# Kernel optimization log

Measured on AMD Instinct MI355X. Metric: run time of the kernel, lower is better.

## Reference

```python
import jax, jax.numpy as jnp
import numpy as np

HIDDEN = 2048
NUM_HEADS = 16
HEAD_DIM = HIDDEN // NUM_HEADS
ROPE_THETA = 10000.0
B, S = 2, 2048
NEG_INF = jnp.finfo(jnp.float32).min


def _rope_tables(seq_len, head_dim, base):
    inv_freq = 1.0 / (base ** (jnp.arange(0, head_dim, 2, dtype=jnp.float32) / head_dim))
    t = jnp.arange(seq_len, dtype=jnp.float32)
    freqs = jnp.outer(t, inv_freq)                 # [S, head_dim/2]
    emb = jnp.concatenate([freqs, freqs], axis=-1) # [S, head_dim]
    return jnp.cos(emb), jnp.sin(emb)


def _rotate_half(x):
    x1, x2 = jnp.split(x, 2, axis=-1)
    return jnp.concatenate([-x2, x1], axis=-1)


def _apply_rope(q, k, cos, sin, position_ids):
    # q,k: [B,H,S,D]; cos/sin: [S_max,D]; position_ids: [B,S]
    c = cos[position_ids][:, None, :, :]  # [B,1,S,D]
    s = sin[position_ids][:, None, :, :]
    q = q * c + _rotate_half(q) * s
    k = k * c + _rotate_half(k) * s
    return q, k


def setup_inputs() -> dict:
    key = jax.random.key(0)
    ks = jax.random.split(key, 5)
    hidden_states = jax.random.normal(ks[0], (B, S, HIDDEN), dtype=jnp.float32)
    # causal additive mask, shape (B,1,S,S)
    causal = jnp.triu(jnp.full((S, S), NEG_INF, dtype=jnp.float32), k=1)
    attention_mask = jnp.broadcast_to(causal[None, None], (B, 1, S, S))
    position_ids = jnp.broadcast_to(jnp.arange(S, dtype=jnp.int32)[None], (B, S))
    scale = 1.0 / np.sqrt(HIDDEN)
    Wq = jax.random.normal(ks[1], (HIDDEN, HIDDEN), dtype=jnp.float32) * scale
    Wk = jax.random.normal(ks[2], (HIDDEN, HIDDEN), dtype=jnp.float32) * scale
    Wv = jax.random.normal(ks[3], (HIDDEN, HIDDEN), dtype=jnp.float32) * scale
    Wo = jax.random.normal(ks[4], (HIDDEN, HIDDEN), dtype=jnp.float32) * scale
    return {"hidden_states": hidden_states, "attention_mask": attention_mask,
            "position_ids": position_ids, "Wq": Wq, "Wk": Wk, "Wv": Wv, "Wo": Wo}


def reference(hidden_states, attention_mask, position_ids, Wq, Wk, Wv, Wo):
    bsz, q_len, _ = hidden_states.shape
    def proj(W):
        # nn.Linear: x @ W.T -> [B,S,H*D] -> [B,H,S,D]
        y = jnp.einsum('bse,fe->bsf', hidden_states, W)
        return y.reshape(bsz, q_len, NUM_HEADS, HEAD_DIM).transpose(0, 2, 1, 3)
    q, k, v = proj(Wq), proj(Wk), proj(Wv)
    cos, sin = _rope_tables(q_len, HEAD_DIM, ROPE_THETA)
    q, k = _apply_rope(q, k, cos, sin, position_ids)
    scores = jnp.einsum('bhqd,bhkd->bhqk', q, k) / np.sqrt(HEAD_DIM)
    scores = scores + attention_mask
    scores = jnp.maximum(scores, NEG_INF)
    weights = jax.nn.softmax(scores.astype(jnp.float32), axis=-1).astype(q.dtype)
    attn = jnp.einsum('bhqk,bhkd->bhqd', weights, v)
    attn = attn.transpose(0, 2, 1, 3).reshape(bsz, q_len, HIDDEN)
    return jnp.einsum('bsf,ef->bse', attn, Wo)
```

## Files before the change

kernel.cpp:

```cpp
#include <hip/hip_runtime.h>
#include <hip/hip_bf16.h>

typedef __attribute__((ext_vector_type(4))) float f32x4;
typedef __attribute__((ext_vector_type(8))) short bf16x8;
typedef __attribute__((ext_vector_type(4))) unsigned u32x4;

__device__ __forceinline__ short f2b(float f) {
  unsigned u = __builtin_bit_cast(unsigned, f);
  u += 0x7FFFu + ((u >> 16) & 1u);
  return (short)(u >> 16);
}
__device__ __forceinline__ float b2f(short s) {
  unsigned u = ((unsigned)(unsigned short)s) << 16;
  return __builtin_bit_cast(float, u);
}
__device__ __forceinline__ unsigned cvtpk(float lo, float hi) {
  unsigned r;
  asm("v_cvt_pk_bf16_f32 %0, %1, %2" : "=v"(r) : "v"(lo), "v"(hi));
  return r;
}

__device__ __forceinline__ void async16(const void* g, void* l) {
  __builtin_amdgcn_global_load_lds(
      (const __attribute__((address_space(1))) void*)g,
      (__attribute__((address_space(3))) void*)l, 16, 0, 0);
}

#define BM 128
#define BN 128
#define BK 64

__global__ __launch_bounds__(256) void cvt_kernel(
    const float* __restrict__ X, const float* __restrict__ Wq,
    const float* __restrict__ Wk, const float* __restrict__ Wv,
    const float* __restrict__ Wo, short* __restrict__ dst) {
  const size_t u = (size_t)blockIdx.x * 256 + threadIdx.x;
  const float* src;
  short* d;
  size_t off;
  if (u < 1048576) {
    src = X; d = dst; off = u * 8;
  } else {
    const size_t j = u - 1048576;
    const int ten = (int)(j >> 19);
    off = (j & 524287) * 8;
    src = (ten == 0) ? Wq : (ten == 1) ? Wk : (ten == 2) ? Wv : Wo;
    d = dst + 8388608 + (size_t)ten * 4194304;
  }
  const f32x4 lo = *(const f32x4*)(src + off);
  const f32x4 hi = *(const f32x4*)(src + off + 4);
  bf16x8 v;
#pragma unroll
  for (int i = 0; i < 4; ++i) { v[i] = f2b(lo[i]); v[i + 4] = f2b(hi[i]); }
  *(bf16x8*)(d + off) = v;
}

template <int MODE>
__global__ __launch_bounds__(256, 2) void gemm_kernel(
    const short* __restrict__ A,
    const short* __restrict__ B0,
    const short* __restrict__ B1,
    const short* __restrict__ B2,
    void* __restrict__ O0,
    short* __restrict__ O1,
    short* __restrict__ O2) {
  constexpr int K = 2048;
  const int m0 = blockIdx.x * BM;
  const int n0 = blockIdx.y * BN;
  const short* B;
  if (MODE == 0) {
    const int wsel = blockIdx.z;
    B = (wsel == 0) ? B0 : ((wsel == 1) ? B1 : B2);
  } else {
    B = B0;
  }

  __shared__ __align__(16) short As[BM * BK];
  __shared__ __align__(16) short Bs[BN * BK];

  const int t = threadIdx.x;
  const int wave = t >> 6;
  const int lane = t & 63;
  const int qd = lane >> 4;
  const int ln = lane & 15;
  const int wr = wave >> 1;
  const int wc = wave & 1;

  const f32x4 zero = {0.f, 0.f, 0.f, 0.f};
  f32x4 acc[4][4];
#pragma unroll
  for (int i = 0; i < 4; ++i)
#pragma unroll
    for (int j = 0; j < 4; ++j) acc[i][j] = zero;

  const int srow = t >> 3;
  const int sgp = (t & 7) ^ (srow & 7);
  const short* Ag = A + (size_t)(m0 + srow) * K + sgp * 8;
  const short* Bg = B + (size_t)(n0 + srow) * K + sgp * 8;
  short* Asw = &As[wave * 512];
  short* Bsw = &Bs[wave * 512];

  for (int k0 = 0; k0 < K; k0 += BK) {
    __syncthreads();
#pragma unroll
    for (int r = 0; r < 4; ++r) {
      async16(Ag + (size_t)(r * 32) * K + k0, Asw + r * 2048);
      async16(Bg + (size_t)(r * 32) * K + k0, Bsw + r * 2048);
    }
    __syncthreads();

    bf16x8 af[2][4], bf[2][4];
#pragma unroll
    for (int kc = 0; kc < 2; ++kc) {
#pragma unroll
      for (int i = 0; i < 4; ++i) {
        const int m = wr * 64 + i * 16 + ln;
        af[kc][i] = *(const bf16x8*)&As[m * BK + (((kc * 4 + qd) ^ (m & 7)) << 3)];
        const int n = wc * 64 + i * 16 + ln;
        bf[kc][i] = *(const bf16x8*)&Bs[n * BK + (((kc * 4 + qd) ^ (n & 7)) << 3)];
      }
    }
#pragma unroll
    for (int kc = 0; kc < 2; ++kc)
#pragma unroll
      for (int i = 0; i < 4; ++i)
#pragma unroll
        for (int j = 0; j < 4; ++j)
          acc[i][j] = __builtin_amdgcn_mfma_f32_16x16x32_bf16(af[kc][i], bf[kc][j],
                                                              acc[i][j], 0, 0, 0);
  }

#pragma unroll
  for (int i = 0; i < 4; ++i) {
#pragma unroll
    for (int j = 0; j < 4; ++j) {
      const int n = n0 + wc * 64 + j * 16 + ln;
#pragma unroll
      for (int rr = 0; rr < 4; ++rr) {
        const int m = m0 + wr * 64 + i * 16 + qd * 4 + rr;
        if (MODE == 1) {
          ((float*)O0)[(size_t)m * 2048 + n] = acc[i][j][rr];
        } else {
          const short v = f2b(acc[i][j][rr]);
          const int b = m >> 11, s = m & 2047;
          const int h = n >> 7, d = n & 127;
          if (blockIdx.z == 0)
            ((short*)O0)[((size_t)(b * 16 + h) * 2048 + s) * 128 + d] = v;
          else if (blockIdx.z == 1)
            O1[((size_t)(b * 16 + h) * 2048 + s) * 128 + d] = v;
          else
            O2[((size_t)(b * 16 + h) * 128 + d) * 2048 + s] = v;
        }
      }
    }
  }
}

__global__ void rope_kernel(short* __restrict__ Q,
                            short* __restrict__ Kb,
                            const int* __restrict__ pos_ids) {
  const int idx = blockIdx.x * 256 + threadIdx.x;
  const int d = idx & 63;
  const int row = idx >> 6;
  const int tsel = row >> 16;
  const int r = row & 65535;
  const int s = r & 2047;
  const int b = r >> 15;
  const int pos = pos_ids[b * 2048 + s];
  const float invf = __builtin_exp2f(-(float)d * 0.20762050593117475f);
  const float ang = (float)pos * invf;
  const float c = cosf(ang), sn = sinf(ang);
  const float qs = tsel ? 1.0f : 0.12751743f;
  short* P = (tsel ? Kb : Q) + (size_t)r * 128;
  const float x1 = b2f(P[d]);
  const float x2 = b2f(P[d + 64]);
  P[d] = f2b((x1 * c - x2 * sn) * qs);
  P[d + 64] = f2b((x2 * c + x1 * sn) * qs);
}

__global__ __launch_bounds__(256, 5) void attn_kernel(
    const short* __restrict__ Q,
    const short* __restrict__ Kbuf,
    const short* __restrict__ Vt,
    short* __restrict__ O) {
  const int n = blockIdx.x;
  const int xcd = n & 7;
  const int m_ = n >> 3;
  const int bh = xcd + 8 * (m_ & 3);
  const int x_ = m_ >> 2;
  const int u_ = x_ & 7;
  const int g_ = x_ >> 3;
  const int qt = (g_ == 0) ? 2 * u_
               : (g_ == 1) ? 31 - 2 * u_
               : (g_ == 2) ? 2 * u_ + 1
                           : 30 - 2 * u_;
  const int q0 = qt * 64;
  const size_t hoff = (size_t)bh * 2048 * 128;
  const short* Qh = Q + hoff;
  const short* Kh = Kbuf + hoff;
  const short* Vh = Vt + hoff;

  __shared__ __align__(16) short Ks[2][32 * 128];
  __shared__ __align__(16) short Vs[2][128 * 32];

  const int t = threadIdx.x;
  const int wave = t >> 6;
  const int lane = t & 63;
  const int qd = lane >> 4;
  const int ln = lane & 15;
  const int qw0 = q0 + wave * 16;

  bf16x8 qf[4];
  {
    const short* qp = Qh + (size_t)(qw0 + ln) * 128 + qd * 8;
#pragma unroll
    for (int kc = 0; kc < 4; ++kc) qf[kc] = *(const bf16x8*)(qp + kc * 32);
  }

  const f32x4 zero = {0.f, 0.f, 0.f, 0.f};
  f32x4 oacc[8];
#pragma unroll
  for (int dt = 0; dt < 8; ++dt) oacc[dt] = zero;
  float mrow = -1e30f;
  float lrow = 0.f;

  const int kr = t >> 4;
  const int gk = (t & 15) ^ (kr & 7);
  const int vr = t >> 2;
  const int gv = (t & 3) ^ (vr & 3) ^ ((vr >> 2) & 3);
  const short* Kg = Kh + (size_t)kr * 128 + gk * 8;
  const short* Vg = Vh + (size_t)vr * 2048 + gv * 8;
  const int wb = wave * 512;

  const int nkv = 2 * qt + 2;

#pragma unroll
  for (int rd = 0; rd < 2; ++rd) {
    async16(Kg + (size_t)(rd * 16) * 128, &Ks[0][rd * 2048 + wb]);
    async16(Vg + (size_t)rd * 131072, &Vs[0][rd * 2048 + wb]);
  }

  int cur = 0;
  for (int kt = 0; kt < nkv; ++kt) {
    const int k0 = kt * 32;
    __syncthreads();
    if (kt + 1 < nkv) {
      const int k1 = k0 + 32;
#pragma unroll
      for (int rd = 0; rd < 2; ++rd) {
        async16(Kg + (size_t)(k1 + rd * 16) * 128, &Ks[cur ^ 1][rd * 2048 + wb]);
        async16(Vg + (size_t)rd * 131072 + k1, &Vs[cur ^ 1][rd * 2048 + wb]);
      }
    }

    if (k0 <= qw0 + 15) {
      const short* Kc = &Ks[cur][0];
      f32x4 sc[2];
#pragma unroll
      for (int j = 0; j < 2; ++j) {
        sc[j] = zero;
        const int krow = j * 16 + ln;
#pragma unroll
        for (int kc = 0; kc < 4; ++kc) {
          const bf16x8 kf =
              *(const bf16x8*)&Kc[krow * 128 + (((kc * 4 + qd) ^ (krow & 7)) << 3)];
          sc[j] = __builtin_amdgcn_mfma_f32_16x16x32_bf16(kf, qf[kc], sc[j], 0, 0, 0);
        }
      }

      float pvv[2][4];
#pragma unroll
      for (int j = 0; j < 2; ++j)
#pragma unroll
        for (int rr = 0; rr < 4; ++rr) pvv[j][rr] = sc[j][rr];
      if (k0 + 31 > qw0) {
        const int qrow = qw0 + ln;
#pragma unroll
        for (int j = 0; j < 2; ++j)
#pragma unroll
          for (int rr = 0; rr < 4; ++rr)
            if (k0 + j * 16 + qd * 4 + rr > qrow) pvv[j][rr] = -1e30f;
      }

      float tmax = pvv[0][0];
#pragma unroll
      for (int j = 0; j < 2; ++j)
#pragma unroll
        for (int rr = 0; rr < 4; ++rr) tmax = fmaxf(tmax, pvv[j][rr]);
      tmax = fmaxf(tmax, __shfl_xor(tmax, 16));
      tmax = fmaxf(tmax, __shfl_xor(tmax, 32));

      if (__any(tmax > mrow + 8.f)) {
        const float mnew = fmaxf(mrow, tmax);
        const float al = __builtin_exp2f(mrow - mnew);
        mrow = mnew;
        lrow *= al;
        float a[4];
#pragma unroll
        for (int rr = 0; rr < 4; ++rr) a[rr] = __shfl(al, qd * 4 + rr);
#pragma unroll
        for (int dt = 0; dt < 8; ++dt)
#pragma unroll
          for (int rr = 0; rr < 4; ++rr) oacc[dt][rr] *= a[rr];
      }

      float ps = 0.f;
#pragma unroll
      for (int j = 0; j < 2; ++j)
#pragma unroll
        for (int rr = 0; rr < 4; ++rr) {
          const float p = __builtin_exp2f(pvv[j][rr] - mrow);
          pvv[j][rr] = p;
          ps += p;
        }
      ps += __shfl_xor(ps, 16);
      ps += __shfl_xor(ps, 32);
      lrow += ps;

      const unsigned A0 = cvtpk(pvv[0][0], pvv[0][1]);
      const unsigned A1 = cvtpk(pvv[0][2], pvv[0][3]);
      const unsigned B0 = cvtpk(pvv[1][0], pvv[1][1]);
      const unsigned B1 = cvtpk(pvv[1][2], pvv[1][3]);
      const int s0 = ln + ((qd & 1) << 5);
      const int s1 = s0 + 16;
      const unsigned a0 = __shfl(A0, s0), a1 = __shfl(A1, s0);
      const unsigned a2 = __shfl(A0, s1), a3 = __shfl(A1, s1);
      const unsigned b0 = __shfl(B0, s0), b1 = __shfl(B1, s0);
      const unsigned b2 = __shfl(B0, s1), b3 = __shfl(B1, s1);
      const bool useA = (qd < 2);
      u32x4 pr;
      pr[0] = useA ? a0 : b0;
      pr[1] = useA ? a1 : b1;
      pr[2] = useA ? a2 : b2;
      pr[3] = useA ? a3 : b3;
      const bf16x8 pf = __builtin_bit_cast(bf16x8, pr);

      const short* Vc = &Vs[cur][0];
#pragma unroll
      for (int dt = 0; dt < 8; ++dt) {
        const int d = dt * 16 + ln;
        const bf16x8 vf =
            *(const bf16x8*)&Vc[d * 32 + (((qd ^ (d & 3) ^ ((d >> 2) & 3)) << 3))];
        oacc[dt] = __builtin_amdgcn_mfma_f32_16x16x32_bf16(pf, vf, oacc[dt], 0, 0, 0);
      }
    }
    cur ^= 1;
  }

  const int b = bh >> 4;
  const int h = bh & 15;
  float rl[4];
#pragma unroll
  for (int rr = 0; rr < 4; ++rr) rl[rr] = 1.0f / __shfl(lrow, qd * 4 + rr);
#pragma unroll
  for (int dt = 0; dt < 8; ++dt) {
    const int d = dt * 16 + ln;
#pragma unroll
    for (int rr = 0; rr < 4; ++rr) {
      const int q = qw0 + qd * 4 + rr;
      O[((size_t)(b * 2048 + q)) * 2048 + h * 128 + d] = f2b(oacc[dt][rr] * rl[rr]);
    }
  }
}

extern "C" void kernel_launch(void* const* d_in, const int* in_sizes, int n_in,
                              void* d_out, int out_size, void* d_ws, size_t ws_size,
                              hipStream_t stream) {
  const float* X  = (const float*)d_in[0];
  const int* pos  = (const int*)d_in[2];
  const float* Wq = (const float*)d_in[3];
  const float* Wk = (const float*)d_in[4];
  const float* Wv = (const float*)d_in[5];
  const float* Wo = (const float*)d_in[6];
  float* out = (float*)d_out;

  short* ws = (short*)d_ws;
  short* Xb  = ws;
  short* Wqb = ws + 8388608;
  short* Wkb = Wqb + 4194304;
  short* Wvb = Wkb + 4194304;
  short* Wob = Wvb + 4194304;
  short* Qb  = Wob + 4194304;
  short* Kb  = Qb + 8388608;
  short* Vt  = Kb + 8388608;
  short* Ob  = Vt + 8388608;

  cvt_kernel<<<dim3(12288), 256, 0, stream>>>(X, Wq, Wk, Wv, Wo, Xb);
  gemm_kernel<0><<<dim3(32, 16, 3), 256, 0, stream>>>(Xb, Wqb, Wkb, Wvb,
                                                      Qb, Kb, Vt);
  rope_kernel<<<dim3(32768), 256, 0, stream>>>(Qb, Kb, pos);
  attn_kernel<<<dim3(1024), 256, 0, stream>>>(Qb, Kb, Vt, Ob);
  gemm_kernel<1><<<dim3(32, 16, 1), 256, 0, stream>>>(Ob, Wob, nullptr, nullptr,
                                                      out, nullptr, nullptr);
}
```

Measured before the change: 428.7 us.

## Fuse RoPE into QKV projection epilogue with precomputed cos/sin tables

Removes the separate rope kernel. RoPE rotation and the query scaling now run in the Q/K projection GEMM epilogue. The partner half-dimension values are exchanged through shared memory between the wave columns. The cos/sin tables are built once in the conversion kernel using extra blocks. This drops one read-modify-write pass over Q and K in bf16 and a kernel launch, at the cost of extra LDS traffic, syncs and table loads in the GEMM epilogue.

```diff
diff --git a/kernel.cpp b/kernel.cpp
--- a/kernel.cpp
+++ b/kernel.cpp
@@ -33,8 +33,18 @@
 __global__ __launch_bounds__(256) void cvt_kernel(
     const float* __restrict__ X, const float* __restrict__ Wq,
     const float* __restrict__ Wk, const float* __restrict__ Wv,
-    const float* __restrict__ Wo, short* __restrict__ dst) {
+    const float* __restrict__ Wo, short* __restrict__ dst,
+    float* __restrict__ Tc, float* __restrict__ Ts) {
   const size_t u = (size_t)blockIdx.x * 256 + threadIdx.x;
+  if (u >= 3145728) {
+    const int idx = (int)(u - 3145728);
+    const int pos = idx >> 6, d = idx & 63;
+    const float invf = __builtin_exp2f(-(float)d * 0.20762050593117475f);
+    const float ang = (float)pos * invf;
+    Tc[idx] = cosf(ang);
+    Ts[idx] = sinf(ang);
+    return;
+  }
   const float* src;
   short* d;
   size_t off;
@@ -63,7 +73,10 @@
     const short* __restrict__ B2,
     void* __restrict__ O0,
     short* __restrict__ O1,
-    short* __restrict__ O2) {
+    short* __restrict__ O2,
+    const int* __restrict__ pos_ids,
+    const float* __restrict__ Tc,
+    const float* __restrict__ Ts) {
   constexpr int K = 2048;
   const int m0 = blockIdx.x * BM;
   const int n0 = blockIdx.y * BN;
@@ -130,52 +143,66 @@
                                                               acc[i][j], 0, 0, 0);
   }
 
-#pragma unroll
-  for (int i = 0; i < 4; ++i) {
-#pragma unroll
-    for (int j = 0; j < 4; ++j) {
-      const int n = n0 + wc * 64 + j * 16 + ln;
-#pragma unroll
-      for (int rr = 0; rr < 4; ++rr) {
-        const int m = m0 + wr * 64 + i * 16 + qd * 4 + rr;
-        if (MODE == 1) {
-          ((float*)O0)[(size_t)m * 2048 + n] = acc[i][j][rr];
-        } else {
-          const short v = f2b(acc[i][j][rr]);
+  if (MODE == 0 && blockIdx.z != 2) {
+    float* fx = (float*)As;
+    const float qs = (blockIdx.z == 0) ? 0.12751743f : 1.0f;
+    short* Od = (blockIdx.z == 0) ? (short*)O0 : O1;
+    const int h = n0 >> 7;
+    const int pt = t ^ 64;
+#pragma unroll
+    for (int round = 0; round < 2; ++round) {
+      __syncthreads();
+#pragma unroll
+      for (int ii = 0; ii < 2; ++ii)
+#pragma unroll
+        for (int j = 0; j < 4; ++j)
+#pragma unroll
+          for (int rr = 0; rr < 4; ++rr)
+            fx[(ii * 16 + j * 4 + rr) * 256 + t] = acc[round * 2 + ii][j][rr];
+      __syncthreads();
+#pragma unroll
+      for (int ii = 0; ii < 2; ++ii) {
+        const int i = round * 2 + ii;
+#pragma unroll
+        for (int rr = 0; rr < 4; ++rr) {
+          const int m = m0 + wr * 64 + i * 16 + qd * 4 + rr;
           const int b = m >> 11, s = m & 2047;
-          const int h = n >> 7, d = n & 127;
-          if (blockIdx.z == 0)
-            ((short*)O0)[((size_t)(b * 16 + h) * 2048 + s) * 128 + d] = v;
-          else if (blockIdx.z == 1)
-            O1[((size_t)(b * 16 + h) * 2048 + s) * 128 + d] = v;
-          else
+          const int pos = pos_ids[b * 2048 + s];
+#pragma unroll
+          for (int j = 0; j < 4; ++j) {
+            const int dd = j * 16 + ln;
+            const float c = Tc[pos * 64 + dd];
+            const float sn = Ts[pos * 64 + dd];
+            const float x = acc[i][j][rr];
+            const float xp = fx[(ii * 16 + j * 4 + rr) * 256 + pt];
+            const float val = wc ? (x * c + xp * sn) : (x * c - xp * sn);
+            const int d = wc * 64 + dd;
+            Od[((size_t)(b * 16 + h) * 2048 + s) * 128 + d] = f2b(val * qs);
+          }
+        }
+      }
+    }
+  } else {
+#pragma unroll
+    for (int i = 0; i < 4; ++i) {
+#pragma unroll
+      for (int j = 0; j < 4; ++j) {
+        const int n = n0 + wc * 64 + j * 16 + ln;
+#pragma unroll
+        for (int rr = 0; rr < 4; ++rr) {
+          const int m = m0 + wr * 64 + i * 16 + qd * 4 + rr;
+          if (MODE == 1) {
+            ((float*)O0)[(size_t)m * 2048 + n] = acc[i][j][rr];
+          } else {
+            const short v = f2b(acc[i][j][rr]);
+            const int b = m >> 11, s = m & 2047;
+            const int h = n >> 7, d = n & 127;
             O2[((size_t)(b * 16 + h) * 128 + d) * 2048 + s] = v;
+          }
         }
       }
     }
   }
-}
-
-__global__ void rope_kernel(short* __restrict__ Q,
-                            short* __restrict__ Kb,
-                            const int* __restrict__ pos_ids) {
-  const int idx = blockIdx.x * 256 + threadIdx.x;
-  const int d = idx & 63;
-  const int row = idx >> 6;
-  const int tsel = row >> 16;
-  const int r = row & 65535;
-  const int s = r & 2047;
-  const int b = r >> 15;
-  const int pos = pos_ids[b * 2048 + s];
-  const float invf = __builtin_exp2f(-(float)d * 0.20762050593117475f);
-  const float ang = (float)pos * invf;
-  const float c = cosf(ang), sn = sinf(ang);
-  const float qs = tsel ? 1.0f : 0.12751743f;
-  short* P = (tsel ? Kb : Q) + (size_t)r * 128;
-  const float x1 = b2f(P[d]);
-  const float x2 = b2f(P[d + 64]);
-  P[d] = f2b((x1 * c - x2 * sn) * qs);
-  P[d + 64] = f2b((x2 * c + x1 * sn) * qs);
 }
 
 __global__ __launch_bounds__(256, 5) void attn_kernel(
@@ -384,12 +411,14 @@
   short* Kb  = Qb + 8388608;
   short* Vt  = Kb + 8388608;
   short* Ob  = Vt + 8388608;
-
-  cvt_kernel<<<dim3(12288), 256, 0, stream>>>(X, Wq, Wk, Wv, Wo, Xb);
+  float* Tc  = (float*)(Ob + 8388608);
+  float* Ts  = Tc + 131072;
+
+  cvt_kernel<<<dim3(12800), 256, 0, stream>>>(X, Wq, Wk, Wv, Wo, Xb, Tc, Ts);
   gemm_kernel<0><<<dim3(32, 16, 3), 256, 0, stream>>>(Xb, Wqb, Wkb, Wvb,
-                                                      Qb, Kb, Vt);
-  rope_kernel<<<dim3(32768), 256, 0, stream>>>(Qb, Kb, pos);
+                                                      Qb, Kb, Vt, pos, Tc, Ts);
   attn_kernel<<<dim3(1024), 256, 0, stream>>>(Qb, Kb, Vt, Ob);
   gemm_kernel<1><<<dim3(32, 16, 1), 256, 0, stream>>>(Ob, Wob, nullptr, nullptr,
-                                                      out, nullptr, nullptr);
-}
+                                                      out, nullptr, nullptr,
+                                                      nullptr, nullptr, nullptr);
+}
```

After: 396.7 us. 7.4% less time.
